# Kernel tuning notes

Measured on AMD Instinct MI355X. Metric: run time of the kernel, lower is better.

Reference implementation:

```python
import jax, jax.numpy as jnp
import numpy as np

B, C, L = 32, 8, 2048
K, S = 512, 64  # num_shapelets, shapelets_size


def setup_inputs() -> dict:
    key = jax.random.key(0)
    k1, k2 = jax.random.split(key)
    x = jax.random.normal(k1, (B, C, L), dtype=jnp.float32)
    shapelets = jax.random.normal(k2, (C, K, S), dtype=jnp.float32)
    return {"x": x, "shapelets": shapelets}


def reference(x, shapelets):
    # x: [B, C, L]; shapelets: [C, K, S]
    s = shapelets.shape[-1]
    n_dims = x.shape[1]
    W = x.shape[2] - s + 1  # number of sliding windows
    # unfold(2, S, 1): gather overlapping windows -> [B, C, W, S]
    idx = jnp.arange(W)[:, None] + jnp.arange(s)[None, :]
    xw = x[:, :, idx]
    # L2-normalize windows along window length (clamp min like torch)
    xw = xw / jnp.maximum(jnp.linalg.norm(xw, axis=-1, keepdims=True), 1e-8)
    # L2-normalize shapelets along length
    sn = shapelets / jnp.maximum(jnp.linalg.norm(shapelets, axis=-1, keepdims=True), 1e-8)
    # matmul [B,C,W,S] @ [C,S,K] then sum over C, fused into one einsum -> [B, W, K]
    sim = jnp.einsum('bcws,cks->bwk', xw, sn) / n_dims
    sim = jax.nn.relu(sim)
    # max over window positions -> [B, K]; keep the singleton channel dim like torch ([B,1,K])
    out = jnp.max(sim, axis=1)
    return out[:, None, :]
```

## Files before the change

### kernel.cpp

```cpp
#include <hip/hip_runtime.h>


#define B_ 32
#define C_ 8
#define L_ 2048
#define K_ 512
#define S_ 64
#define W_ (L_ - S_ + 1)
#define TW 64
#define NWT ((W_ + TW - 1) / TW)
#define XP 128

typedef _Float16 f16x8 __attribute__((ext_vector_type(8)));
typedef float f32x4 __attribute__((ext_vector_type(4)));

__global__ __launch_bounds__(64)
void pack_sn_k(const float* __restrict__ sh, _Float16* __restrict__ Bp) {
    const int blk  = blockIdx.x;
    const int c    = blk >> 6;
    const int ks   = (blk >> 5) & 1;
    const int nt   = blk & 31;
    const int lane = threadIdx.x;
    const int ncol = lane & 15, quad = lane >> 4;
    const int q    = nt * 16 + ncol;

    const float4* sp = (const float4*)(sh + (size_t)(c * K_ + q) * S_);
    float ss = 0.f;
    #pragma unroll
    for (int i = 0; i < 4; ++i) {
        float4 v = sp[quad * 4 + i];
        ss += v.x * v.x + v.y * v.y + v.z * v.z + v.w * v.w;
    }
    ss += __shfl_xor(ss, 16);
    ss += __shfl_xor(ss, 32);
    float inv = 1.f / fmaxf(sqrtf(ss), 1e-8f);

    float4 u0 = sp[ks * 8 + quad * 2];
    float4 u1 = sp[ks * 8 + quad * 2 + 1];
    f16x8 o;
    o[0] = (_Float16)(u0.x * inv); o[1] = (_Float16)(u0.y * inv);
    o[2] = (_Float16)(u0.z * inv); o[3] = (_Float16)(u0.w * inv);
    o[4] = (_Float16)(u1.x * inv); o[5] = (_Float16)(u1.y * inv);
    o[6] = (_Float16)(u1.z * inv); o[7] = (_Float16)(u1.w * inv);
    ((f16x8*)Bp)[((c * 2 + ks) * 32 + nt) * 64 + lane] = o;
}

__global__ __launch_bounds__(256, 2)
void mcs_mfma_k(const float* __restrict__ x, const _Float16* __restrict__ Bp,
                float* __restrict__ out) {
    __shared__ float xl[C_ * XP];
    __shared__ float invn[C_ * TW];

    const int wt  = blockIdx.x;
    const int b   = blockIdx.y;
    const int w0  = wt * TW;
    const int tid = threadIdx.x;

    for (int i = tid; i < C_ * XP; i += 256) {
        int c = i >> 7, p = i & 127;
        int pos = w0 + p;
        float v = 0.f;
        if (p < 127 && pos < L_) v = x[(size_t)(b * C_ + c) * L_ + pos];
        xl[i] = v;
    }
    __syncthreads();

    for (int t = tid; t < C_ * TW; t += 256) {
        int c = t >> 6, m = t & 63;
        const float* p = xl + c * XP + m;
        float s0 = 0.f, s1 = 0.f, s2 = 0.f, s3 = 0.f;
        #pragma unroll
        for (int j = 0; j < S_; j += 4) {
            s0 += p[j] * p[j];     s1 += p[j + 1] * p[j + 1];
            s2 += p[j + 2] * p[j + 2]; s3 += p[j + 3] * p[j + 3];
        }
        float ss = (s0 + s1) + (s2 + s3);
        invn[t] = 0.125f / fmaxf(sqrtf(ss), 1e-8f);
    }
    __syncthreads();

    const int lane = tid & 63;
    const int wid  = tid >> 6;
    const int row  = lane & 15;
    const int quad = lane >> 4;
    const int ntb  = wid * 8;

    f32x4 acc[4][8];
    #pragma unroll
    for (int mt = 0; mt < 4; ++mt)
        #pragma unroll
        for (int nt = 0; nt < 8; ++nt)
            acc[mt][nt] = (f32x4){0.f, 0.f, 0.f, 0.f};

    #pragma unroll 1
    for (int c = 0; c < C_; ++c) {
        float iv[4];
        #pragma unroll
        for (int mt = 0; mt < 4; ++mt) iv[mt] = invn[c * TW + mt * 16 + row];

        #pragma unroll
        for (int ks = 0; ks < 2; ++ks) {
            f16x8 afr[4];
            #pragma unroll
            for (int mt = 0; mt < 4; ++mt) {
                const float* p = xl + c * XP + mt * 16 + row + ks * 32 + quad * 8;
                #pragma unroll
                for (int j = 0; j < 8; ++j)
                    afr[mt][j] = (_Float16)(p[j] * iv[mt]);
            }
            const f16x8* bpp = (const f16x8*)Bp + ((c * 2 + ks) * 32 + ntb) * 64 + lane;
            f16x8 bfr[8];
            #pragma unroll
            for (int nt = 0; nt < 8; ++nt) bfr[nt] = bpp[nt * 64];

            #pragma unroll
            for (int nt = 0; nt < 8; ++nt)
                #pragma unroll
                for (int mt = 0; mt < 4; ++mt)
                    acc[mt][nt] = __builtin_amdgcn_mfma_f32_16x16x32_f16(
                        afr[mt], bfr[nt], acc[mt][nt], 0, 0, 0);
        }
    }

    #pragma unroll
    for (int nt = 0; nt < 8; ++nt) {
        float m = 0.f;
        #pragma unroll
        for (int mt = 0; mt < 4; ++mt) {
            #pragma unroll
            for (int r = 0; r < 4; ++r) {
                int w = w0 + mt * 16 + quad * 4 + r;
                if (w < W_) m = fmaxf(m, acc[mt][nt][r]);
            }
        }
        m = fmaxf(m, __shfl_xor(m, 16));
        m = fmaxf(m, __shfl_xor(m, 32));
        if (lane < 16)
            atomicMax((unsigned int*)(out + b * K_ + (ntb + nt) * 16 + lane),
                      __float_as_uint(m));
    }
}

extern "C" void kernel_launch(void* const* d_in, const int* in_sizes, int n_in,
                              void* d_out, int out_size, void* d_ws, size_t ws_size,
                              hipStream_t stream) {
    const float* x  = (const float*)d_in[0];
    const float* sh = (const float*)d_in[1];
    float* out = (float*)d_out;
    _Float16* Bp = (_Float16*)d_ws;

    hipMemsetAsync(out, 0, (size_t)out_size * sizeof(float), stream);
    pack_sn_k<<<dim3(512), dim3(64), 0, stream>>>(sh, Bp);
    mcs_mfma_k<<<dim3(NWT, B_), dim3(256), 0, stream>>>(x, Bp, out);
}
```

Baseline: 99.89 us.

## Double window tile, stage normalized fp16 A fragments in LDS, fold memset into pack

Each block now covers 128 windows with 512 threads in two wave groups, so every B fragment load serves twice as many windows. Window norms are computed cooperatively per channel pair and the normalized fp16 A fragments are written once to shared memory, instead of each wave re-converting from fp32 LDS. The output zeroing moves into the pack kernel, which drops the separate memset launch. The cost is more LDS, extra barriers per phase, and higher register pressure at 512 threads per block.

```diff
diff --git a/kernel.cpp b/kernel.cpp
--- a/kernel.cpp
+++ b/kernel.cpp
@@ -7,20 +7,25 @@
 #define K_ 512
 #define S_ 64
 #define W_ (L_ - S_ + 1)
-#define TW 64
+#define TW 128
 #define NWT ((W_ + TW - 1) / TW)
-#define XP 128
+#define XP 192
 
 typedef _Float16 f16x8 __attribute__((ext_vector_type(8)));
 typedef float f32x4 __attribute__((ext_vector_type(4)));
 
-__global__ __launch_bounds__(64)
-void pack_sn_k(const float* __restrict__ sh, _Float16* __restrict__ Bp) {
-    const int blk  = blockIdx.x;
+__global__ __launch_bounds__(256)
+void pack_sn_k(const float* __restrict__ sh, _Float16* __restrict__ Bp,
+               float* __restrict__ out) {
+    const int tid = threadIdx.x;
+    int gid = blockIdx.x * 256 + tid;
+    if (gid < B_ * K_) out[gid] = 0.f;
+
+    const int blk  = blockIdx.x * 4 + (tid >> 6);
     const int c    = blk >> 6;
     const int ks   = (blk >> 5) & 1;
     const int nt   = blk & 31;
-    const int lane = threadIdx.x;
+    const int lane = tid & 63;
     const int ncol = lane & 15, quad = lane >> 4;
     const int q    = nt * 16 + ncol;
 
@@ -45,45 +50,37 @@
     ((f16x8*)Bp)[((c * 2 + ks) * 32 + nt) * 64 + lane] = o;
 }
 
-__global__ __launch_bounds__(256, 2)
+__global__ __launch_bounds__(512, 2)
 void mcs_mfma_k(const float* __restrict__ x, const _Float16* __restrict__ Bp,
                 float* __restrict__ out) {
     __shared__ float xl[C_ * XP];
-    __shared__ float invn[C_ * TW];
+    __shared__ f16x8 AhV[32 * 64];
+    __shared__ float psum[512];
 
     const int wt  = blockIdx.x;
     const int b   = blockIdx.y;
     const int w0  = wt * TW;
     const int tid = threadIdx.x;
 
-    for (int i = tid; i < C_ * XP; i += 256) {
-        int c = i >> 7, p = i & 127;
+    for (int i = tid; i < C_ * XP; i += 512) {
+        int c = i / XP, p = i - c * XP;
         int pos = w0 + p;
         float v = 0.f;
-        if (p < 127 && pos < L_) v = x[(size_t)(b * C_ + c) * L_ + pos];
+        if (p < 191 && pos < L_) v = x[(size_t)(b * C_ + c) * L_ + pos];
         xl[i] = v;
     }
-    __syncthreads();
-
-    for (int t = tid; t < C_ * TW; t += 256) {
-        int c = t >> 6, m = t & 63;
-        const float* p = xl + c * XP + m;
-        float s0 = 0.f, s1 = 0.f, s2 = 0.f, s3 = 0.f;
-        #pragma unroll
-        for (int j = 0; j < S_; j += 4) {
-            s0 += p[j] * p[j];     s1 += p[j + 1] * p[j + 1];
-            s2 += p[j + 2] * p[j + 2]; s3 += p[j + 3] * p[j + 3];
-        }
-        float ss = (s0 + s1) + (s2 + s3);
-        invn[t] = 0.125f / fmaxf(sqrtf(ss), 1e-8f);
-    }
-    __syncthreads();
 
     const int lane = tid & 63;
     const int wid  = tid >> 6;
+    const int g    = wid >> 2;
+    const int nw   = wid & 3;
     const int row  = lane & 15;
     const int quad = lane >> 4;
-    const int ntb  = wid * 8;
+
+    const int r_  = tid & 255;
+    const int h_  = tid >> 8;
+    const int cc_ = r_ >> 7;
+    const int w_  = r_ & 127;
 
     f32x4 acc[4][8];
     #pragma unroll
@@ -93,32 +90,62 @@
             acc[mt][nt] = (f32x4){0.f, 0.f, 0.f, 0.f};
 
     #pragma unroll 1
-    for (int c = 0; c < C_; ++c) {
-        float iv[4];
-        #pragma unroll
-        for (int mt = 0; mt < 4; ++mt) iv[mt] = invn[c * TW + mt * 16 + row];
+    for (int ph = 0; ph < 4; ++ph) {
+        const int c0 = ph * 2;
+        __syncthreads();
+
+        float xv[32];
+        {
+            const float* xp = xl + (c0 + cc_) * XP + w_ + h_ * 32;
+            float s0 = 0.f, s1 = 0.f, s2 = 0.f, s3 = 0.f;
+            #pragma unroll
+            for (int i = 0; i < 32; i += 4) {
+                xv[i] = xp[i]; xv[i+1] = xp[i+1];
+                xv[i+2] = xp[i+2]; xv[i+3] = xp[i+3];
+                s0 += xv[i]*xv[i];     s1 += xv[i+1]*xv[i+1];
+                s2 += xv[i+2]*xv[i+2]; s3 += xv[i+3]*xv[i+3];
+            }
+            psum[tid] = (s0 + s1) + (s2 + s3);
+        }
+        __syncthreads();
+        {
+            float sst = psum[r_] + psum[r_ + 256];
+            float inv = 0.125f / fmaxf(sqrtf(sst), 1e-8f);
+            const int fb = (cc_ * 2 + h_) * 8 + (w_ >> 4);
+            #pragma unroll
+            for (int qd = 0; qd < 4; ++qd) {
+                f16x8 o;
+                #pragma unroll
+                for (int j = 0; j < 8; ++j)
+                    o[j] = (_Float16)(xv[qd * 8 + j] * inv);
+                AhV[fb * 64 + qd * 16 + (w_ & 15)] = o;
+            }
+        }
+        __syncthreads();
 
         #pragma unroll
-        for (int ks = 0; ks < 2; ++ks) {
-            f16x8 afr[4];
+        for (int cc = 0; cc < 2; ++cc) {
             #pragma unroll
-            for (int mt = 0; mt < 4; ++mt) {
-                const float* p = xl + c * XP + mt * 16 + row + ks * 32 + quad * 8;
-                #pragma unroll
-                for (int j = 0; j < 8; ++j)
-                    afr[mt][j] = (_Float16)(p[j] * iv[mt]);
-            }
-            const f16x8* bpp = (const f16x8*)Bp + ((c * 2 + ks) * 32 + ntb) * 64 + lane;
-            f16x8 bfr[8];
-            #pragma unroll
-            for (int nt = 0; nt < 8; ++nt) bfr[nt] = bpp[nt * 64];
-
-            #pragma unroll
-            for (int nt = 0; nt < 8; ++nt)
+            for (int ks = 0; ks < 2; ++ks) {
+                f16x8 af[4];
+                const int fb = (cc * 2 + ks) * 8 + g * 4;
                 #pragma unroll
                 for (int mt = 0; mt < 4; ++mt)
-                    acc[mt][nt] = __builtin_amdgcn_mfma_f32_16x16x32_f16(
-                        afr[mt], bfr[nt], acc[mt][nt], 0, 0, 0);
+                    af[mt] = AhV[(fb + mt) * 64 + lane];
+
+                const f16x8* bpp = (const f16x8*)Bp +
+                    (((c0 + cc) * 2 + ks) * 32 + nw * 8) * 64 + lane;
+                f16x8 bf[8];
+                #pragma unroll
+                for (int nt = 0; nt < 8; ++nt) bf[nt] = bpp[nt * 64];
+
+                #pragma unroll
+                for (int nt = 0; nt < 8; ++nt)
+                    #pragma unroll
+                    for (int mt = 0; mt < 4; ++mt)
+                        acc[mt][nt] = __builtin_amdgcn_mfma_f32_16x16x32_f16(
+                            af[mt], bf[nt], acc[mt][nt], 0, 0, 0);
+            }
         }
     }
 
@@ -128,15 +155,15 @@
         #pragma unroll
         for (int mt = 0; mt < 4; ++mt) {
             #pragma unroll
-            for (int r = 0; r < 4; ++r) {
-                int w = w0 + mt * 16 + quad * 4 + r;
-                if (w < W_) m = fmaxf(m, acc[mt][nt][r]);
+            for (int rr = 0; rr < 4; ++rr) {
+                int w = w0 + g * 64 + mt * 16 + quad * 4 + rr;
+                if (w < W_) m = fmaxf(m, acc[mt][nt][rr]);
             }
         }
         m = fmaxf(m, __shfl_xor(m, 16));
         m = fmaxf(m, __shfl_xor(m, 32));
         if (lane < 16)
-            atomicMax((unsigned int*)(out + b * K_ + (ntb + nt) * 16 + lane),
+            atomicMax((unsigned int*)(out + b * K_ + (nw * 8 + nt) * 16 + lane),
                       __float_as_uint(m));
     }
 }
@@ -149,7 +176,6 @@
     float* out = (float*)d_out;
     _Float16* Bp = (_Float16*)d_ws;
 
-    hipMemsetAsync(out, 0, (size_t)out_size * sizeof(float), stream);
-    pack_sn_k<<<dim3(512), dim3(64), 0, stream>>>(sh, Bp);
-    mcs_mfma_k<<<dim3(NWT, B_), dim3(256), 0, stream>>>(x, Bp, out);
+    pack_sn_k<<<dim3(128), dim3(256), 0, stream>>>(sh, Bp, out);
+    mcs_mfma_k<<<dim3(NWT, B_), dim3(512), 0, stream>>>(x, Bp, out);
 }
```

Result: slower. 103.1 us (+3.2%).
